# Kernel tuning notes

Measured on AMD Instinct MI355X. Metric: run time of the kernel, lower is better.

## Reference

```python
import jax, jax.numpy as jnp
import numpy as np


def setup_inputs() -> dict:
    key = jax.random.key(0)
    ks = jax.random.split(key, 6)
    B, S, F, U = 64, 1024, 1024, 1024
    scale = 0.02
    return {
        "features": jax.random.normal(ks[0], (B, S, F), dtype=jnp.float32),
        "hidden": jax.random.normal(ks[1], (B, U), dtype=jnp.float32),
        "W1_w": jax.random.normal(ks[2], (F, U), dtype=jnp.float32) * scale,
        "W1_b": jnp.zeros((U,), dtype=jnp.float32),
        "W2_w": jax.random.normal(ks[3], (U, U), dtype=jnp.float32) * scale,
        "W2_b": jnp.zeros((U,), dtype=jnp.float32),
        "V_w": jax.random.normal(ks[4], (U, 1), dtype=jnp.float32) * scale,
        "V_b": jnp.zeros((1,), dtype=jnp.float32),
    }


def reference(features, hidden, W1_w, W1_b, W2_w, W2_b, V_w, V_b):
    # features: [B, S, F]; hidden: [B, H]
    # score = tanh(W1(features) + W2(hidden)[:, None, :])  -> [B, S, U]
    proj_f = jnp.einsum("bsf,fu->bsu", features, W1_w) + W1_b
    proj_h = hidden @ W2_w + W2_b  # [B, U]
    score = jnp.tanh(proj_f + proj_h[:, None, :])
    # logits: [B, S, 1]; softmax over seq axis (axis=1)
    logits = jnp.einsum("bsu,uo->bso", score, V_w) + V_b
    attention_weights = jax.nn.softmax(logits, axis=1)
    # context: sum over seq of weights * features -> [B, F]
    context_vector = jnp.sum(attention_weights * features, axis=1)
    return context_vector, attention_weights
```

## Files before the change

### kernel.cpp

```cpp
#include <hip/hip_runtime.h>
#include <hip/hip_bf16.h>
#include <stdint.h>

#define B_ 64
#define S_ 1024
#define F_ 1024
#define U_ 1024
#define M_ (B_*S_)

typedef __attribute__((ext_vector_type(4))) float  f4;
typedef __attribute__((ext_vector_type(4))) float  f32x4;
typedef __attribute__((ext_vector_type(8))) short  short8;
typedef unsigned int u32;

static __device__ __forceinline__ short f2bf(float x){
    union { float f; uint32_t u; } v; v.f = x;
    uint32_t u = v.u;
    u += 0x7fffu + ((u >> 16) & 1u);
    return (short)(u >> 16);
}

static __device__ __forceinline__ void glds16(const void* g, void* l){
    __builtin_amdgcn_global_load_lds(
        (const __attribute__((address_space(1))) u32*)g,
        (__attribute__((address_space(3))) u32*)l, 16, 0, 0);
}

static __device__ __forceinline__ float fast_tanh(float x){
    float e = __expf(2.f * x);
    return 1.f - 2.f / (e + 1.f);
}

__global__ void pack_w1(const float* __restrict__ W1, short* __restrict__ Bws){
    int g = blockIdx.x * 256 + threadIdx.x;
    int n    =  g        & 127;
    int kgrp = (g >> 7)  & 3;
    int nb   = (g >> 9)  & 7;
    int kb   =  g >> 12;
    int u  = nb*128 + n;
    int f0 = kb*32 + kgrp*8;
    short8 o;
#pragma unroll
    for (int j = 0; j < 8; ++j)
        o[j] = f2bf(W1[(size_t)(f0 + j)*U_ + u]);
    *(short8*)&Bws[(size_t)g * 8] = o;
}

__global__ void hb_kernel(const float* __restrict__ hidden, const float* __restrict__ W2,
                          const float* __restrict__ W2b, const float* __restrict__ W1b,
                          float* __restrict__ hb){
    __shared__ float hs[U_];
    int b = blockIdx.y, t = threadIdx.x;
    for (int i = t; i < U_; i += 256) hs[i] = hidden[b*U_ + i];
    __syncthreads();
    int u = blockIdx.x*256 + t;
    float acc = W1b[u] + W2b[u];
#pragma unroll 8
    for (int k = 0; k < U_; ++k)
        acc = fmaf(hs[k], W2[(size_t)k*U_ + u], acc);
    hb[b*U_ + u] = acc;
}

__global__ __launch_bounds__(256) void gemm_score(
        const float* __restrict__ A, const short* __restrict__ Bws,
        const float* __restrict__ hb, const float* __restrict__ Vw,
        float* __restrict__ logits){
    __shared__ short Abuf[4096];
    __shared__ short Bbuf[2][4096];

    const int t   = threadIdx.x;
    const int bid = blockIdx.x;
    const int mb = bid >> 3, nb = bid & 7;
    const int m0 = mb*128,  n0 = nb*128;
    const int batch = m0 >> 10;
    const int w = t >> 6, l = t & 63;
    const int wr = w >> 1, wc = w & 1;
    const int kg = l >> 4, fr = l & 15;
    const int ar = t >> 1, ah = t & 1;

    const float* aptr = A + (size_t)(m0 + ar)*F_ + ah*16;

    f32x4 acc[4][4];
#pragma unroll
    for (int i = 0; i < 4; ++i)
#pragma unroll
        for (int j = 0; j < 4; ++j) acc[i][j] = (f32x4)0.f;

    f4 a0 = *(const f4*)(aptr + 0);
    f4 a1 = *(const f4*)(aptr + 4);
    f4 a2 = *(const f4*)(aptr + 8);
    f4 a3 = *(const f4*)(aptr + 12);
    {
        const char* src = (const char*)Bws + ((size_t)(0*8 + nb) << 13) + (w<<11) + (l<<4);
        char* dst = (char*)&Bbuf[0][0] + (w<<11);
        glds16(src, dst);
        glds16(src + 1024, dst + 1024);
    }

    for (int kt = 0; kt < 32; ++kt){
        const int sel = kt & 1;
        short8 s0, s1;
        s0[0]=f2bf(a0[0]); s0[1]=f2bf(a0[1]); s0[2]=f2bf(a0[2]); s0[3]=f2bf(a0[3]);
        s0[4]=f2bf(a1[0]); s0[5]=f2bf(a1[1]); s0[6]=f2bf(a1[2]); s0[7]=f2bf(a1[3]);
        s1[0]=f2bf(a2[0]); s1[1]=f2bf(a2[1]); s1[2]=f2bf(a2[2]); s1[3]=f2bf(a2[3]);
        s1[4]=f2bf(a3[0]); s1[5]=f2bf(a3[1]); s1[6]=f2bf(a3[2]); s1[7]=f2bf(a3[3]);
        *(short8*)&Abuf[((2*ah+0)*128 + ar)*8] = s0;
        *(short8*)&Abuf[((2*ah+1)*128 + ar)*8] = s1;
        __syncthreads();

        if (kt < 31){
            const float* ap = aptr + (kt+1)*32;
            a0 = *(const f4*)(ap + 0);
            a1 = *(const f4*)(ap + 4);
            a2 = *(const f4*)(ap + 8);
            a3 = *(const f4*)(ap + 12);
            const char* src = (const char*)Bws + ((size_t)((kt+1)*8 + nb) << 13) + (w<<11) + (l<<4);
            char* dst = (char*)&Bbuf[sel^1][0] + (w<<11);
            glds16(src, dst);
            glds16(src + 1024, dst + 1024);
        }

        short8 af[4], bfr[4];
#pragma unroll
        for (int i = 0; i < 4; ++i)
            af[i] = *(const short8*)&Abuf[(kg*128 + wr*64 + i*16 + fr)*8];
#pragma unroll
        for (int j = 0; j < 4; ++j)
            bfr[j] = *(const short8*)&Bbuf[sel][(kg*128 + wc*64 + j*16 + fr)*8];
#pragma unroll
        for (int i = 0; i < 4; ++i)
#pragma unroll
            for (int j = 0; j < 4; ++j)
                acc[i][j] = __builtin_amdgcn_mfma_f32_16x16x32_bf16(af[i], bfr[j], acc[i][j], 0, 0, 0);
        __syncthreads();
    }

    float hv[4], vv[4];
#pragma unroll
    for (int j = 0; j < 4; ++j){
        int u = n0 + wc*64 + j*16 + fr;
        hv[j] = hb[batch*U_ + u];
        vv[j] = Vw[u];
    }
#pragma unroll
    for (int i = 0; i < 4; ++i){
#pragma unroll
        for (int reg = 0; reg < 4; ++reg){
            float sum = 0.f;
#pragma unroll
            for (int j = 0; j < 4; ++j){
                float sc = fast_tanh(acc[i][j][reg] + hv[j]);
                sum = fmaf(vv[j], sc, sum);
            }
            sum += __shfl_xor(sum, 1, 64);
            sum += __shfl_xor(sum, 2, 64);
            sum += __shfl_xor(sum, 4, 64);
            sum += __shfl_xor(sum, 8, 64);
            if (fr == 0)
                atomicAdd(&logits[m0 + wr*64 + i*16 + kg*4 + reg], sum);
        }
    }
}

__global__ void softmax_seq(float* __restrict__ lg){
    __shared__ float red[4], red2[4];
    int b = blockIdx.x, t = threadIdx.x;
    float v[4];
#pragma unroll
    for (int c = 0; c < 4; ++c) v[c] = lg[b*1024 + c*256 + t];
    float mx = fmaxf(fmaxf(v[0], v[1]), fmaxf(v[2], v[3]));
#pragma unroll
    for (int off = 32; off >= 1; off >>= 1) mx = fmaxf(mx, __shfl_xor(mx, off, 64));
    if ((t & 63) == 0) red[t >> 6] = mx;
    __syncthreads();
    mx = fmaxf(fmaxf(red[0], red[1]), fmaxf(red[2], red[3]));
    float e[4], s = 0.f;
#pragma unroll
    for (int c = 0; c < 4; ++c){ e[c] = __expf(v[c] - mx); s += e[c]; }
#pragma unroll
    for (int off = 32; off >= 1; off >>= 1) s += __shfl_xor(s, off, 64);
    if ((t & 63) == 0) red2[t >> 6] = s;
    __syncthreads();
    s = red2[0] + red2[1] + red2[2] + red2[3];
    float inv = 1.f / s;
#pragma unroll
    for (int c = 0; c < 4; ++c) lg[b*1024 + c*256 + t] = e[c] * inv;
}

__global__ void context_kernel(const float* __restrict__ feats, const float* __restrict__ wts,
                               float* __restrict__ ctx){
    __shared__ float wsh[256];
    int fb = blockIdx.x, sh = blockIdx.y, b = blockIdx.z;
    int t = threadIdx.x;
    wsh[t] = wts[b*1024 + sh*256 + t];
    __syncthreads();
    int f = fb*256 + t;
    const float* fp = feats + ((size_t)b*1024 + sh*256)*1024 + f;
    float a0 = 0.f, a1 = 0.f, a2 = 0.f, a3 = 0.f;
    for (int s = 0; s < 256; s += 4){
        a0 = fmaf(wsh[s+0], fp[(size_t)(s+0)*1024], a0);
        a1 = fmaf(wsh[s+1], fp[(size_t)(s+1)*1024], a1);
        a2 = fmaf(wsh[s+2], fp[(size_t)(s+2)*1024], a2);
        a3 = fmaf(wsh[s+3], fp[(size_t)(s+3)*1024], a3);
    }
    atomicAdd(&ctx[b*1024 + f], a0 + a1 + a2 + a3);
}

extern "C" void kernel_launch(void* const* d_in, const int* in_sizes, int n_in,
                              void* d_out, int out_size, void* d_ws, size_t ws_size,
                              hipStream_t stream){
    const float* features = (const float*)d_in[0];
    const float* hidden   = (const float*)d_in[1];
    const float* W1w      = (const float*)d_in[2];
    const float* W1b      = (const float*)d_in[3];
    const float* W2w      = (const float*)d_in[4];
    const float* W2b      = (const float*)d_in[5];
    const float* Vw       = (const float*)d_in[6];

    float* out = (float*)d_out;
    float* ctx = out;
    float* att = out + 65536;

    short* Bws = (short*)d_ws;
    float* hb  = (float*)((char*)d_ws + (size_t)2*1024*1024);

    hipMemsetAsync(d_out, 0, (size_t)131072 * sizeof(float), stream);
    pack_w1<<<512, 256, 0, stream>>>(W1w, Bws);
    hb_kernel<<<dim3(4, 64), 256, 0, stream>>>(hidden, W2w, W2b, W1b, hb);
    gemm_score<<<4096, 256, 0, stream>>>(features, Bws, hb, Vw, att);
    softmax_seq<<<64, 256, 0, stream>>>(att);
    context_kernel<<<dim3(4, 4, 64), 256, 0, stream>>>(features, att, ctx);
}
```

Measured before the change: 711.2 us.

## Pre-pack features to bf16, stream both GEMM operands via LDS DMA, retile helpers

Adds a pre-pass that converts features to a pre-tiled bf16 buffer in the workspace. A new GEMM then loads both A and B tiles asynchronously with global_load_lds and double buffering, removing per-thread fp32-to-bf16 conversion from the main loop. It also swizzles block indices so each XCD works on contiguous M blocks. Separately, hb_kernel now handles four batches per W2 load, and the context kernel uses float4 loads across the full feature row. The pre-pass costs an extra full read of features plus a 128MB write, and the fallback path only runs when the workspace is too small.

```diff
diff --git a/kernel.cpp b/kernel.cpp
--- a/kernel.cpp
+++ b/kernel.cpp
@@ -6,7 +6,6 @@
 #define S_ 1024
 #define F_ 1024
 #define U_ 1024
-#define M_ (B_*S_)
 
 typedef __attribute__((ext_vector_type(4))) float  f4;
 typedef __attribute__((ext_vector_type(4))) float  f32x4;
@@ -46,32 +45,148 @@
     *(short8*)&Bws[(size_t)g * 8] = o;
 }
 
+__global__ void pack_feat(const float* __restrict__ F, short* __restrict__ out){
+    int bid = blockIdx.x;
+    int t = threadIdx.x;
+    int half = bid & 1, kt = (bid >> 1) & 31, mb = bid >> 6;
+    int row = half*64 + (t >> 2);
+    int kq  = t & 3;
+    const float* src = F + (size_t)(mb*128 + row)*1024 + kt*32 + kq*8;
+    f4 a = *(const f4*)src;
+    f4 b = *(const f4*)(src + 4);
+    short8 o;
+    o[0]=f2bf(a[0]); o[1]=f2bf(a[1]); o[2]=f2bf(a[2]); o[3]=f2bf(a[3]);
+    o[4]=f2bf(b[0]); o[5]=f2bf(b[1]); o[6]=f2bf(b[2]); o[7]=f2bf(b[3]);
+    *(short8*)&out[(size_t)(mb*32 + kt)*4096 + (kq*128 + row)*8] = o;
+}
+
 __global__ void hb_kernel(const float* __restrict__ hidden, const float* __restrict__ W2,
                           const float* __restrict__ W2b, const float* __restrict__ W1b,
                           float* __restrict__ hb){
-    __shared__ float hs[U_];
-    int b = blockIdx.y, t = threadIdx.x;
-    for (int i = t; i < U_; i += 256) hs[i] = hidden[b*U_ + i];
-    __syncthreads();
-    int u = blockIdx.x*256 + t;
-    float acc = W1b[u] + W2b[u];
-#pragma unroll 8
-    for (int k = 0; k < U_; ++k)
-        acc = fmaf(hs[k], W2[(size_t)k*U_ + u], acc);
-    hb[b*U_ + u] = acc;
-}
-
-__global__ __launch_bounds__(256) void gemm_score(
+    __shared__ float hs[4][1024];
+    int ub = blockIdx.x, bg = blockIdx.y, t = threadIdx.x;
+    for (int i = t; i < 4096; i += 256) ((float*)hs)[i] = hidden[(size_t)bg*4096 + i];
+    __syncthreads();
+    int u = ub*256 + t;
+    float base = W1b[u] + W2b[u];
+    float a0 = 0.f, a1 = 0.f, a2 = 0.f, a3 = 0.f;
+#pragma unroll 4
+    for (int k = 0; k < 1024; ++k){
+        float w = W2[(size_t)k*1024 + u];
+        a0 = fmaf(hs[0][k], w, a0);
+        a1 = fmaf(hs[1][k], w, a1);
+        a2 = fmaf(hs[2][k], w, a2);
+        a3 = fmaf(hs[3][k], w, a3);
+    }
+    hb[(size_t)(bg*4 + 0)*1024 + u] = base + a0;
+    hb[(size_t)(bg*4 + 1)*1024 + u] = base + a1;
+    hb[(size_t)(bg*4 + 2)*1024 + u] = base + a2;
+    hb[(size_t)(bg*4 + 3)*1024 + u] = base + a3;
+}
+
+static __device__ __forceinline__ void swz_mbnb(int bid, int& mb, int& nb){
+    int xcd = bid & 7;
+    int seq = bid >> 3;
+    nb = seq & 7;
+    mb = xcd*64 + (seq >> 3);
+}
+
+__global__ __launch_bounds__(256) void gemm_v2(
+        const short* __restrict__ Abf, const short* __restrict__ Bws,
+        const float* __restrict__ hb, const float* __restrict__ Vw,
+        float* __restrict__ logits){
+    __shared__ short Ab[2][4096];
+    __shared__ short Bb[2][4096];
+
+    const int t = threadIdx.x;
+    int mb, nb; swz_mbnb(blockIdx.x, mb, nb);
+    const int m0 = mb*128, n0 = nb*128;
+    const int batch = m0 >> 10;
+    const int w = t >> 6, l = t & 63;
+    const int wr = w >> 1, wc = w & 1;
+    const int kg = l >> 4, fr = l & 15;
+
+    const char* Asrc = (const char*)Abf + ((size_t)(mb*32) << 13) + (w<<11) + (l<<4);
+    const char* Bsrc = (const char*)Bws + ((size_t)nb << 13) + (w<<11) + (l<<4);
+    char* AdstBase[2] = { (char*)&Ab[0][0] + (w<<11), (char*)&Ab[1][0] + (w<<11) };
+    char* BdstBase[2] = { (char*)&Bb[0][0] + (w<<11), (char*)&Bb[1][0] + (w<<11) };
+
+#define STAGE(sel, kt) do{                                   \
+        const char* as_ = Asrc + ((size_t)(kt) << 13);       \
+        const char* bs_ = Bsrc + ((size_t)(kt) << 16);       \
+        glds16(as_,        AdstBase[sel]);                   \
+        glds16(as_ + 1024, AdstBase[sel] + 1024);            \
+        glds16(bs_,        BdstBase[sel]);                   \
+        glds16(bs_ + 1024, BdstBase[sel] + 1024);            \
+    }while(0)
+
+    f32x4 acc[4][4];
+#pragma unroll
+    for (int i = 0; i < 4; ++i)
+#pragma unroll
+        for (int j = 0; j < 4; ++j) acc[i][j] = (f32x4)0.f;
+
+    STAGE(0, 0);
+    asm volatile("s_waitcnt vmcnt(0)");
+    __syncthreads();
+
+    for (int kt = 0; kt < 32; ++kt){
+        const int sel = kt & 1;
+        if (kt < 31) STAGE(sel ^ 1, kt + 1);
+
+        short8 af[4], bfr[4];
+#pragma unroll
+        for (int i = 0; i < 4; ++i)
+            af[i] = *(const short8*)&Ab[sel][(kg*128 + wr*64 + i*16 + fr)*8];
+#pragma unroll
+        for (int j = 0; j < 4; ++j)
+            bfr[j] = *(const short8*)&Bb[sel][(kg*128 + wc*64 + j*16 + fr)*8];
+#pragma unroll
+        for (int i = 0; i < 4; ++i)
+#pragma unroll
+            for (int j = 0; j < 4; ++j)
+                acc[i][j] = __builtin_amdgcn_mfma_f32_16x16x32_bf16(af[i], bfr[j], acc[i][j], 0, 0, 0);
+        __syncthreads();
+    }
+#undef STAGE
+
+    float hv[4], vv[4];
+#pragma unroll
+    for (int j = 0; j < 4; ++j){
+        int u = n0 + wc*64 + j*16 + fr;
+        hv[j] = hb[batch*U_ + u];
+        vv[j] = Vw[u];
+    }
+#pragma unroll
+    for (int i = 0; i < 4; ++i){
+#pragma unroll
+        for (int reg = 0; reg < 4; ++reg){
+            float sum = 0.f;
+#pragma unroll
+            for (int j = 0; j < 4; ++j){
+                float sc = fast_tanh(acc[i][j][reg] + hv[j]);
+                sum = fmaf(vv[j], sc, sum);
+            }
+            sum += __shfl_xor(sum, 1, 64);
+            sum += __shfl_xor(sum, 2, 64);
+            sum += __shfl_xor(sum, 4, 64);
+            sum += __shfl_xor(sum, 8, 64);
+            if (fr == 0)
+                atomicAdd(&logits[m0 + wr*64 + i*16 + kg*4 + reg], sum);
+        }
+    }
+}
+
+__global__ __launch_bounds__(256) void gemm_fb(
         const float* __restrict__ A, const short* __restrict__ Bws,
         const float* __restrict__ hb, const float* __restrict__ Vw,
         float* __restrict__ logits){
     __shared__ short Abuf[4096];
     __shared__ short Bbuf[2][4096];
 
-    const int t   = threadIdx.x;
-    const int bid = blockIdx.x;
-    const int mb = bid >> 3, nb = bid & 7;
-    const int m0 = mb*128,  n0 = nb*128;
+    const int t = threadIdx.x;
+    int mb, nb; swz_mbnb(blockIdx.x, mb, nb);
+    const int m0 = mb*128, n0 = nb*128;
     const int batch = m0 >> 10;
     const int w = t >> 6, l = t & 63;
     const int wr = w >> 1, wc = w & 1;
@@ -91,7 +206,7 @@
     f4 a2 = *(const f4*)(aptr + 8);
     f4 a3 = *(const f4*)(aptr + 12);
     {
-        const char* src = (const char*)Bws + ((size_t)(0*8 + nb) << 13) + (w<<11) + (l<<4);
+        const char* src = (const char*)Bws + ((size_t)nb << 13) + (w<<11) + (l<<4);
         char* dst = (char*)&Bbuf[0][0] + (w<<11);
         glds16(src, dst);
         glds16(src + 1024, dst + 1024);
@@ -189,21 +304,22 @@
 
 __global__ void context_kernel(const float* __restrict__ feats, const float* __restrict__ wts,
                                float* __restrict__ ctx){
-    __shared__ float wsh[256];
-    int fb = blockIdx.x, sh = blockIdx.y, b = blockIdx.z;
-    int t = threadIdx.x;
-    wsh[t] = wts[b*1024 + sh*256 + t];
-    __syncthreads();
-    int f = fb*256 + t;
-    const float* fp = feats + ((size_t)b*1024 + sh*256)*1024 + f;
-    float a0 = 0.f, a1 = 0.f, a2 = 0.f, a3 = 0.f;
-    for (int s = 0; s < 256; s += 4){
-        a0 = fmaf(wsh[s+0], fp[(size_t)(s+0)*1024], a0);
-        a1 = fmaf(wsh[s+1], fp[(size_t)(s+1)*1024], a1);
-        a2 = fmaf(wsh[s+2], fp[(size_t)(s+2)*1024], a2);
-        a3 = fmaf(wsh[s+3], fp[(size_t)(s+3)*1024], a3);
-    }
-    atomicAdd(&ctx[b*1024 + f], a0 + a1 + a2 + a3);
+    __shared__ float wsh[128];
+    int sh = blockIdx.x, b = blockIdx.y, t = threadIdx.x;
+    if (t < 128) wsh[t] = wts[b*1024 + sh*128 + t];
+    __syncthreads();
+    const f4* fp = (const f4*)(feats + ((size_t)b*1024 + sh*128)*1024) + t;
+    f4 a0 = (f4)0.f, a1 = (f4)0.f, a2 = (f4)0.f, a3 = (f4)0.f;
+    for (int s = 0; s < 128; s += 4){
+        a0 += wsh[s+0] * fp[(size_t)(s+0)*256];
+        a1 += wsh[s+1] * fp[(size_t)(s+1)*256];
+        a2 += wsh[s+2] * fp[(size_t)(s+2)*256];
+        a3 += wsh[s+3] * fp[(size_t)(s+3)*256];
+    }
+    f4 r = (a0 + a1) + (a2 + a3);
+    float* c = ctx + b*1024 + t*4;
+    atomicAdd(c+0, r[0]); atomicAdd(c+1, r[1]);
+    atomicAdd(c+2, r[2]); atomicAdd(c+3, r[3]);
 }
 
 extern "C" void kernel_launch(void* const* d_in, const int* in_sizes, int n_in,
@@ -221,13 +337,23 @@
     float* ctx = out;
     float* att = out + 65536;
 
-    short* Bws = (short*)d_ws;
-    float* hb  = (float*)((char*)d_ws + (size_t)2*1024*1024);
+    short* Bws    = (short*)d_ws;
+    float* hb     = (float*)((char*)d_ws + (size_t)2*1024*1024);
+    short* featbf = (short*)((char*)d_ws + (size_t)2*1024*1024 + 256*1024);
+
+    const size_t need = (size_t)2*1024*1024 + 256*1024 + (size_t)128*1024*1024;
 
     hipMemsetAsync(d_out, 0, (size_t)131072 * sizeof(float), stream);
     pack_w1<<<512, 256, 0, stream>>>(W1w, Bws);
-    hb_kernel<<<dim3(4, 64), 256, 0, stream>>>(hidden, W2w, W2b, W1b, hb);
-    gemm_score<<<4096, 256, 0, stream>>>(features, Bws, hb, Vw, att);
+    hb_kernel<<<dim3(4, 16), 256, 0, stream>>>(hidden, W2w, W2b, W1b, hb);
+
+    if (ws_size >= need){
+        pack_feat<<<32768, 256, 0, stream>>>(features, featbf);
+        gemm_v2<<<4096, 256, 0, stream>>>(featbf, Bws, hb, Vw, att);
+    } else {
+        gemm_fb<<<4096, 256, 0, stream>>>(features, Bws, hb, Vw, att);
+    }
+
     softmax_seq<<<64, 256, 0, stream>>>(att);
-    context_kernel<<<dim3(4, 4, 64), 256, 0, stream>>>(features, att, ctx);
-}
+    context_kernel<<<dim3(8, 64), 256, 0, stream>>>(features, att, ctx);
+}
```

Result: slower. 762.1 us (+7.2%).
